# Performance work log

Hardware: AMD Instinct MI355X
Metric: run time of the kernel (lower is better)

The kernel has to match this reference:

```python
import jax, jax.numpy as jnp
import numpy as np


def setup_inputs() -> dict:
    key = jax.random.key(0)
    k1, k2, k3 = jax.random.split(key, 3)
    B, E, L, D = 32, 256, 2048, 256
    doc_state = jax.random.normal(k1, (B, L, D), dtype=jnp.float32)
    entity_mapping = jax.random.uniform(k2, (B, E, L), dtype=jnp.float32)
    entity_lens = jax.random.uniform(k3, (B, E), dtype=jnp.float32)
    return {"doc_state": doc_state, "entity_mapping": entity_mapping, "entity_lens": entity_lens}


def reference(doc_state, entity_mapping, entity_lens):
    # Original: (entity_mapping[:, :, :, None] * doc_state[:, None, :, :]).sum(2) / entity_lens[:, :, None]
    # This is a batched contraction over L; express as einsum to avoid the
    # huge [B, E, L, D] intermediate.
    summed = jnp.einsum('bel,bld->bed', entity_mapping, doc_state)  # [B, E, D]
    return summed / entity_lens[:, :, None]
```

## Files before the change

### kernel.cpp

```cpp
#include <hip/hip_runtime.h>
#include <stdint.h>

#define B_ 32
#define E_ 256
#define L_ 2048
#define D_ 256

#define BE 64
#define BD 64
#define BK 64
#define KS 4
#define KCHUNK (L_ / KS)
#define NKT (KCHUNK / BK)

#define SLAB_FLOATS ((size_t)B_ * E_ * D_)
#define WS_NEED     (KS * SLAB_FLOATS * 4)

typedef __attribute__((ext_vector_type(2))) float  f32x2;
typedef __attribute__((ext_vector_type(4))) float  f32x4;
typedef __attribute__((ext_vector_type(4))) short  s16x4;
typedef __attribute__((ext_vector_type(8))) short  s16x8;

__device__ __forceinline__ void cvt_hilo1(float x, short &h, short &l) {
    unsigned u = __builtin_bit_cast(unsigned, x);
    h = (short)(u >> 16);
    float hf = __builtin_bit_cast(float, u & 0xFFFF0000u);
    unsigned r = __builtin_bit_cast(unsigned, x - hf);
    l = (short)(r >> 16);
}
__device__ __forceinline__ void cvt_hilo4(const f32x4 v, s16x4 &h, s16x4 &l) {
    #pragma unroll
    for (int i = 0; i < 4; ++i) { short hh, ll; cvt_hilo1(v[i], hh, ll); h[i] = hh; l[i] = ll; }
}

__global__ void zero_out_kernel(f32x4* __restrict__ out) {
    out[(size_t)blockIdx.x * 256 + threadIdx.x] = f32x4{0.f, 0.f, 0.f, 0.f};
}

__global__ __launch_bounds__(256)
void reduce_kernel(const f32x4* __restrict__ ws, const float* __restrict__ lens,
                   f32x4* __restrict__ out) {
    const size_t i = (size_t)blockIdx.x * 256 + threadIdx.x;
    const float lv = lens[i >> 6];
    f32x4 s0 = ws[i];
    f32x4 s1 = ws[i +     (SLAB_FLOATS / 4)];
    f32x4 s2 = ws[i + 2 * (SLAB_FLOATS / 4)];
    f32x4 s3 = ws[i + 3 * (SLAB_FLOATS / 4)];
    f32x4 r;
    #pragma unroll
    for (int c = 0; c < 4; ++c) r[c] = (s0[c] + s1[c] + s2[c] + s3[c]) / lv;
    out[i] = r;
}

template <int WS>
__global__ __launch_bounds__(256, 5)
void mean_pool_kernel(const float* __restrict__ doc,
                      const float* __restrict__ emap,
                      const float* __restrict__ lens,
                      float* __restrict__ out,
                      float* __restrict__ wsp) {
    __shared__ __align__(16) short As_hi[BE][BK];
    __shared__ __align__(16) short As_lo[BE][BK];
    __shared__ __align__(16) short Bs_hi[BD][BK];
    __shared__ __align__(16) short Bs_lo[BD][BK];

    const int t   = threadIdx.x;
    const int blk = blockIdx.x;
    const int ks  = blk & 3;
    const int d0  = ((blk >> 2) & 3) * BD;
    const int e0  = ((blk >> 4) & 3) * BE;
    const int b   = blk >> 6;

    const float* Ag = emap + ((size_t)b * E_ + e0) * L_ + ks * KCHUNK;
    const float* Sg = doc  + (size_t)b * L_ * D_ + (size_t)ks * KCHUNK * D_ + d0;

    const int a_c4 = t & 15;
    const int a_r  = t >> 4;
    const int db = t & 31;
    const int kb = t >> 5;

    const int lane = t & 63;
    const int w    = t >> 6;
    const int eo   = (w & 1) * 32;
    const int dq   = (w >> 1) * 32;
    const int ml   = lane & 15;
    const int kg   = lane >> 4;

    f32x4 acc[2][2] = {};
    f32x4 pa[4];
    f32x2 pb[8];

    #pragma unroll
    for (int rr = 0; rr < 4; ++rr)
        pa[rr] = *(const f32x4*)(Ag + (size_t)(a_r + rr * 16) * L_ + a_c4 * 4);
    #pragma unroll
    for (int i = 0; i < 8; ++i)
        pb[i] = *(const f32x2*)(Sg + (size_t)(kb * 8 + i) * D_ + db * 2);

    for (int kt = 0; kt < NKT; ++kt) {
        #pragma unroll
        for (int rr = 0; rr < 4; ++rr) {
            const int row = a_r + rr * 16;
            s16x4 h, l;
            cvt_hilo4(pa[rr], h, l);
            const int col = (((a_c4 >> 1) ^ (row & 7)) << 3) + (a_c4 & 1) * 4;
            *(s16x4*)&As_hi[row][col] = h;
            *(s16x4*)&As_lo[row][col] = l;
        }
        #pragma unroll
        for (int dd = 0; dd < 2; ++dd) {
            const int row = db * 2 + dd;
            s16x8 h, l;
            #pragma unroll
            for (int j = 0; j < 8; ++j) {
                short hh, ll; cvt_hilo1(pb[j][dd], hh, ll);
                h[j] = hh; l[j] = ll;
            }
            const int key = (db & 3) | (((db >> 2) & 1) << 2);
            const int col = (kb ^ key) << 3;
            *(s16x8*)&Bs_hi[row][col] = h;
            *(s16x8*)&Bs_lo[row][col] = l;
        }
        __syncthreads();

        if (kt + 1 < NKT) {
            const int k0 = (kt + 1) * BK;
            #pragma unroll
            for (int rr = 0; rr < 4; ++rr)
                pa[rr] = *(const f32x4*)(Ag + (size_t)(a_r + rr * 16) * L_ + k0 + a_c4 * 4);
            #pragma unroll
            for (int i = 0; i < 8; ++i)
                pb[i] = *(const f32x2*)(Sg + (size_t)(k0 + kb * 8 + i) * D_ + db * 2);
        }

        #pragma unroll
        for (int kc = 0; kc < 2; ++kc) {
            const int gbase = kc * 4;
            s16x8 ah[2], al[2], bh[2], bl[2];
            #pragma unroll
            for (int mi = 0; mi < 2; ++mi) {
                const int row = eo + mi * 16 + ml;
                const int col = ((gbase + kg) ^ (row & 7)) << 3;
                ah[mi] = *(const s16x8*)&As_hi[row][col];
                al[mi] = *(const s16x8*)&As_lo[row][col];
            }
            #pragma unroll
            for (int ni = 0; ni < 2; ++ni) {
                const int row = dq + ni * 16 + ml;
                const int keyB = ((row >> 1) & 3) | (((row >> 3) & 1) << 2);
                const int col  = ((gbase + kg) ^ keyB) << 3;
                bh[ni] = *(const s16x8*)&Bs_hi[row][col];
                bl[ni] = *(const s16x8*)&Bs_lo[row][col];
            }
            #pragma unroll
            for (int mi = 0; mi < 2; ++mi)
                #pragma unroll
                for (int ni = 0; ni < 2; ++ni) {
                    acc[mi][ni] = __builtin_amdgcn_mfma_f32_16x16x32_bf16(ah[mi], bh[ni], acc[mi][ni], 0, 0, 0);
                    acc[mi][ni] = __builtin_amdgcn_mfma_f32_16x16x32_bf16(ah[mi], bl[ni], acc[mi][ni], 0, 0, 0);
                    acc[mi][ni] = __builtin_amdgcn_mfma_f32_16x16x32_bf16(al[mi], bh[ni], acc[mi][ni], 0, 0, 0);
                }
        }
        __syncthreads();
    }

    if (WS) {
        float* wsb = wsp + (size_t)ks * SLAB_FLOATS;
        #pragma unroll
        for (int mi = 0; mi < 2; ++mi) {
            #pragma unroll
            for (int rr = 0; rr < 4; ++rr) {
                const int er = eo + mi * 16 + kg * 4 + rr;
                #pragma unroll
                for (int ni = 0; ni < 2; ++ni)
                    wsb[((size_t)(b * E_ + e0 + er)) * D_ + d0 + dq + ni * 16 + ml] =
                        acc[mi][ni][rr];
            }
        }
    } else {
        __shared__ float lens_s[BE];
        if (t < BE) lens_s[t] = lens[b * E_ + e0 + t];
        __syncthreads();
        #pragma unroll
        for (int mi = 0; mi < 2; ++mi) {
            #pragma unroll
            for (int rr = 0; rr < 4; ++rr) {
                const int er = eo + mi * 16 + kg * 4 + rr;
                const float lv = lens_s[er];
                #pragma unroll
                for (int ni = 0; ni < 2; ++ni)
                    atomicAdd(&out[((size_t)(b * E_ + e0 + er)) * D_ + d0 + dq + ni * 16 + ml],
                              acc[mi][ni][rr] / lv);
            }
        }
    }
}

extern "C" void kernel_launch(void* const* d_in, const int* in_sizes, int n_in,
                              void* d_out, int out_size, void* d_ws, size_t ws_size,
                              hipStream_t stream) {
    const float* doc  = (const float*)d_in[0];
    const float* emap = (const float*)d_in[1];
    const float* lens = (const float*)d_in[2];
    float* out = (float*)d_out;
    float* ws  = (float*)d_ws;

    dim3 grid(B_ * (E_ / BE) * (D_ / BD) * KS);
    dim3 block(256);

    if (ws_size >= (size_t)WS_NEED) {
        hipLaunchKernelGGL((mean_pool_kernel<1>), grid, block, 0, stream,
                           doc, emap, lens, out, ws);
        hipLaunchKernelGGL(reduce_kernel,
                           dim3((unsigned)(SLAB_FLOATS / 4 / 256)), dim3(256), 0, stream,
                           (const f32x4*)ws, lens, (f32x4*)out);
    } else {
        zero_out_kernel<<<dim3(out_size / (4 * 256)), dim3(256), 0, stream>>>((f32x4*)out);
        hipLaunchKernelGGL((mean_pool_kernel<0>), grid, block, 0, stream,
                           doc, emap, lens, out, ws);
    }
}
```

Measured before the change: 171.4 us.

## Halve split-K, pack bf16 pairs with v_perm, and use LDS-only barriers

Split-K is reduced from 4 to 2 chunks, which halves the workspace writes and the reads in the reduce kernel, while each block runs twice as many K iterations. The hi/lo bf16 conversion now packs pairs with v_perm_b32 to cut ALU instructions. __syncthreads is replaced by a barrier that waits only on lgkmcnt, so next-tile global prefetches issued before the barrier are not drained. The barrier sits after the prefetch issue, which lets those loads overlap with the MFMA section. The cost is fewer blocks (4096 instead of 8192) to hide latency.

```diff
diff --git a/kernel.cpp b/kernel.cpp
--- a/kernel.cpp
+++ b/kernel.cpp
@@ -9,28 +9,30 @@
 #define BE 64
 #define BD 64
 #define BK 64
-#define KS 4
+#define KS 2
 #define KCHUNK (L_ / KS)
 #define NKT (KCHUNK / BK)
 
 #define SLAB_FLOATS ((size_t)B_ * E_ * D_)
 #define WS_NEED     (KS * SLAB_FLOATS * 4)
 
-typedef __attribute__((ext_vector_type(2))) float  f32x2;
-typedef __attribute__((ext_vector_type(4))) float  f32x4;
-typedef __attribute__((ext_vector_type(4))) short  s16x4;
-typedef __attribute__((ext_vector_type(8))) short  s16x8;
-
-__device__ __forceinline__ void cvt_hilo1(float x, short &h, short &l) {
-    unsigned u = __builtin_bit_cast(unsigned, x);
-    h = (short)(u >> 16);
-    float hf = __builtin_bit_cast(float, u & 0xFFFF0000u);
-    unsigned r = __builtin_bit_cast(unsigned, x - hf);
-    l = (short)(r >> 16);
-}
-__device__ __forceinline__ void cvt_hilo4(const f32x4 v, s16x4 &h, s16x4 &l) {
-    #pragma unroll
-    for (int i = 0; i < 4; ++i) { short hh, ll; cvt_hilo1(v[i], hh, ll); h[i] = hh; l[i] = ll; }
+typedef __attribute__((ext_vector_type(2))) float    f32x2;
+typedef __attribute__((ext_vector_type(4))) float    f32x4;
+typedef __attribute__((ext_vector_type(8))) short    s16x8;
+typedef __attribute__((ext_vector_type(2))) unsigned u32x2;
+typedef __attribute__((ext_vector_type(4))) unsigned u32x4;
+
+__device__ __forceinline__ unsigned pack_hi_pair(float x0, float x1) {
+    return __builtin_amdgcn_perm(__builtin_bit_cast(unsigned, x1),
+                                 __builtin_bit_cast(unsigned, x0), 0x07060302u);
+}
+__device__ __forceinline__ unsigned pack_lo_pair(float x0, float x1) {
+    unsigned u0 = __builtin_bit_cast(unsigned, x0);
+    unsigned u1 = __builtin_bit_cast(unsigned, x1);
+    float l0 = x0 - __builtin_bit_cast(float, u0 & 0xFFFF0000u);
+    float l1 = x1 - __builtin_bit_cast(float, u1 & 0xFFFF0000u);
+    return __builtin_amdgcn_perm(__builtin_bit_cast(unsigned, l1),
+                                 __builtin_bit_cast(unsigned, l0), 0x07060302u);
 }
 
 __global__ void zero_out_kernel(f32x4* __restrict__ out) {
@@ -43,14 +45,19 @@
     const size_t i = (size_t)blockIdx.x * 256 + threadIdx.x;
     const float lv = lens[i >> 6];
     f32x4 s0 = ws[i];
-    f32x4 s1 = ws[i +     (SLAB_FLOATS / 4)];
-    f32x4 s2 = ws[i + 2 * (SLAB_FLOATS / 4)];
-    f32x4 s3 = ws[i + 3 * (SLAB_FLOATS / 4)];
+    f32x4 s1 = ws[i + (SLAB_FLOATS / 4)];
     f32x4 r;
     #pragma unroll
-    for (int c = 0; c < 4; ++c) r[c] = (s0[c] + s1[c] + s2[c] + s3[c]) / lv;
+    for (int c = 0; c < 4; ++c) r[c] = (s0[c] + s1[c]) / lv;
     out[i] = r;
 }
+
+#define LGKM_BARRIER()                                                         \
+    {                                                                          \
+        asm volatile("s_waitcnt lgkmcnt(0)" ::: "memory");                     \
+        __builtin_amdgcn_s_barrier();                                          \
+        asm volatile("" ::: "memory");                                         \
+    }
 
 template <int WS>
 __global__ __launch_bounds__(256, 5)
@@ -66,10 +73,10 @@
 
     const int t   = threadIdx.x;
     const int blk = blockIdx.x;
-    const int ks  = blk & 3;
-    const int d0  = ((blk >> 2) & 3) * BD;
-    const int e0  = ((blk >> 4) & 3) * BE;
-    const int b   = blk >> 6;
+    const int ks  = blk & 1;
+    const int d0  = ((blk >> 1) & 3) * BD;
+    const int e0  = ((blk >> 3) & 3) * BE;
+    const int b   = blk >> 5;
 
     const float* Ag = emap + ((size_t)b * E_ + e0) * L_ + ks * KCHUNK;
     const float* Sg = doc  + (size_t)b * L_ * D_ + (size_t)ks * KCHUNK * D_ + d0;
@@ -101,27 +108,29 @@
         #pragma unroll
         for (int rr = 0; rr < 4; ++rr) {
             const int row = a_r + rr * 16;
-            s16x4 h, l;
-            cvt_hilo4(pa[rr], h, l);
             const int col = (((a_c4 >> 1) ^ (row & 7)) << 3) + (a_c4 & 1) * 4;
-            *(s16x4*)&As_hi[row][col] = h;
-            *(s16x4*)&As_lo[row][col] = l;
+            u32x2 h, l;
+            h[0] = pack_hi_pair(pa[rr][0], pa[rr][1]);
+            h[1] = pack_hi_pair(pa[rr][2], pa[rr][3]);
+            l[0] = pack_lo_pair(pa[rr][0], pa[rr][1]);
+            l[1] = pack_lo_pair(pa[rr][2], pa[rr][3]);
+            *(u32x2*)&As_hi[row][col] = h;
+            *(u32x2*)&As_lo[row][col] = l;
         }
         #pragma unroll
         for (int dd = 0; dd < 2; ++dd) {
             const int row = db * 2 + dd;
-            s16x8 h, l;
-            #pragma unroll
-            for (int j = 0; j < 8; ++j) {
-                short hh, ll; cvt_hilo1(pb[j][dd], hh, ll);
-                h[j] = hh; l[j] = ll;
-            }
             const int key = (db & 3) | (((db >> 2) & 1) << 2);
             const int col = (kb ^ key) << 3;
-            *(s16x8*)&Bs_hi[row][col] = h;
-            *(s16x8*)&Bs_lo[row][col] = l;
-        }
-        __syncthreads();
+            u32x4 h, l;
+            #pragma unroll
+            for (int p = 0; p < 4; ++p) {
+                h[p] = pack_hi_pair(pb[2 * p][dd], pb[2 * p + 1][dd]);
+                l[p] = pack_lo_pair(pb[2 * p][dd], pb[2 * p + 1][dd]);
+            }
+            *(u32x4*)&Bs_hi[row][col] = h;
+            *(u32x4*)&Bs_lo[row][col] = l;
+        }
 
         if (kt + 1 < NKT) {
             const int k0 = (kt + 1) * BK;
@@ -132,6 +141,7 @@
             for (int i = 0; i < 8; ++i)
                 pb[i] = *(const f32x2*)(Sg + (size_t)(k0 + kb * 8 + i) * D_ + db * 2);
         }
+        LGKM_BARRIER();
 
         #pragma unroll
         for (int kc = 0; kc < 2; ++kc) {
@@ -161,7 +171,7 @@
                     acc[mi][ni] = __builtin_amdgcn_mfma_f32_16x16x32_bf16(al[mi], bh[ni], acc[mi][ni], 0, 0, 0);
                 }
         }
-        __syncthreads();
+        LGKM_BARRIER();
     }
 
     if (WS) {
```

New measurement: 171.8 us. No clear change (+0.2%).
